# Kernel tuning notes

Hardware: AMD Instinct MI355X
Metric: run time of the kernel (lower is better)

Reference implementation:

```python
import jax, jax.numpy as jnp
import numpy as np

IN_CH, OUT_CH, HID, NHEAD = 4, 1, 256, 8
VDIM = HID // NHEAD
LOCALITIES = (2.0, 10.0, 10.0, 10.0, 10.0, 200.0)
N_BLOCKS = len(LOCALITIES) - 2
INPUT_RES, LATENT_RES, OUTPUT_RES = (64, 64), (32, 32), (64, 64)
BATCH = 8


def pairwise_dist(res1x, res1y, res2x, res2y):
    gx1 = jnp.linspace(0, 1, res1x + 1)[:-1]
    gy1 = jnp.linspace(0, 1, res1y + 1)[:-1]
    g1x, g1y = jnp.meshgrid(gx1, gy1, indexing='xy')
    grid1 = jnp.stack([g1x.flatten(), g1y.flatten()], axis=-1)
    gx2 = jnp.linspace(0, 1, res2x + 1)[:-1]
    gy2 = jnp.linspace(0, 1, res2y + 1)[:-1]
    g2x, g2y = jnp.meshgrid(gx2, gy2, indexing='xy')
    grid2 = jnp.stack([g2x.flatten(), g2y.flatten()], axis=-1)
    diff = grid1[:, None, :] - grid2[None, :, :]
    return (jnp.sum(diff ** 2, axis=-1) / 2.0).astype(jnp.float32)


def pos_att(m_dist, x, r, w, locality):
    # m_dist:[Nq,Nk]  x:[B,Nk,HID]  r:[H,1,1]  w:[H,HID,VDIM]
    scale = jnp.tan(0.25 * jnp.pi * (1 - 1e-07) * (1 + jnp.sin(r)))
    sd = m_dist[None, :, :] * scale  # [H,Nq,Nk]
    if locality <= 100:
        thr = jnp.percentile(sd, locality, axis=-1, keepdims=True)
        sd = jnp.where(sd <= thr, sd, jnp.inf)
    att = jax.nn.softmax(-sd, axis=-1)  # [H,Nq,Nk]
    value = jnp.einsum('bnj,hjk->bhnk', x, w)  # [B,H,Nk,VDIM]
    out = jnp.einsum('hjn,bhnk->bhjk', att, value)  # [B,H,Nq,VDIM]
    out = jnp.transpose(out, (0, 2, 1, 3)).reshape(x.shape[0], m_dist.shape[0], -1)
    return jax.nn.gelu(out)


def lin(x, w, b):
    # eqx.nn.Linear: w:[out,in], b:[out]
    return jnp.einsum('bni,oi->bno', x, w) + b


def setup_inputs() -> dict:
    key = jax.random.key(0)
    ks = jax.random.split(key, 20)
    Ni = INPUT_RES[0] * INPUT_RES[1]
    s_h = 1.0 / jnp.sqrt(HID)
    s_in = 1.0 / jnp.sqrt(IN_CH)
    return {
        'x': jax.random.normal(ks[0], (BATCH, Ni, IN_CH), jnp.float32),
        'en_fc1_w': jax.random.uniform(ks[1], (HID, IN_CH), jnp.float32, -s_in, s_in),
        'en_fc1_b': jax.random.uniform(ks[2], (HID,), jnp.float32, -s_in, s_in),
        'down_r': jax.random.normal(ks[3], (NHEAD, 1, 1), jnp.float32),
        'down_w': jax.random.normal(ks[4], (NHEAD, HID, VDIM), jnp.float32) * s_h,
        'pa_r': jax.random.normal(ks[5], (N_BLOCKS, NHEAD, 1, 1), jnp.float32),
        'pa_w': jax.random.normal(ks[6], (N_BLOCKS, NHEAD, HID, VDIM), jnp.float32) * s_h,
        'mlp1_w': jax.random.uniform(ks[7], (N_BLOCKS, HID, HID), jnp.float32, -s_h, s_h),
        'mlp1_b': jax.random.uniform(ks[8], (N_BLOCKS, HID), jnp.float32, -s_h, s_h),
        'mlp2_w': jax.random.uniform(ks[9], (N_BLOCKS, HID, HID), jnp.float32, -s_h, s_h),
        'mlp2_b': jax.random.uniform(ks[10], (N_BLOCKS, HID), jnp.float32, -s_h, s_h),
        'res_w': jax.random.uniform(ks[11], (N_BLOCKS, HID, HID), jnp.float32, -s_h, s_h),
        'res_b': jax.random.uniform(ks[12], (N_BLOCKS, HID), jnp.float32, -s_h, s_h),
        'up_r': jax.random.normal(ks[13], (NHEAD, 1, 1), jnp.float32),
        'up_w': jax.random.normal(ks[14], (NHEAD, HID, VDIM), jnp.float32) * s_h,
        'de_fc1_w': jax.random.uniform(ks[15], (HID, HID), jnp.float32, -s_h, s_h),
        'de_fc1_b': jax.random.uniform(ks[16], (HID,), jnp.float32, -s_h, s_h),
        'de_fc2_w': jax.random.uniform(ks[17], (OUT_CH, HID), jnp.float32, -s_h, s_h),
        'de_fc2_b': jax.random.uniform(ks[18], (OUT_CH,), jnp.float32, -s_h, s_h),
    }


def reference(x, en_fc1_w, en_fc1_b, down_r, down_w, pa_r, pa_w,
              mlp1_w, mlp1_b, mlp2_w, mlp2_b, res_w, res_b,
              up_r, up_w, de_fc1_w, de_fc1_b, de_fc2_w, de_fc2_b):
    m_dist_down = pairwise_dist(LATENT_RES[0], LATENT_RES[1], INPUT_RES[0], INPUT_RES[1])
    m_dist_proc = pairwise_dist(LATENT_RES[0], LATENT_RES[1], LATENT_RES[0], LATENT_RES[1])
    m_dist_up = pairwise_dist(OUTPUT_RES[0], OUTPUT_RES[1], LATENT_RES[0], LATENT_RES[1])

    h = jax.nn.gelu(lin(x, en_fc1_w, en_fc1_b))
    h = pos_att(m_dist_down, h, down_r, down_w, LOCALITIES[0])
    for i in range(N_BLOCKS):
        pa_out = pos_att(m_dist_proc, h, pa_r[i], pa_w[i], LOCALITIES[1 + i])
        mlp_out = lin(jax.nn.gelu(lin(pa_out, mlp1_w[i], mlp1_b[i])), mlp2_w[i], mlp2_b[i])
        residual = lin(h, res_w[i], res_b[i])
        h = jax.nn.gelu(mlp_out + residual)
    h = pos_att(m_dist_up, h, up_r, up_w, LOCALITIES[-1])
    h = jax.nn.gelu(lin(h, de_fc1_w, de_fc1_b))
    return lin(h, de_fc2_w, de_fc2_b)
```

## Files before the change

kernel.cpp:

```cpp
#include <hip/hip_runtime.h>
#include <math.h>


#define PI_F 3.14159265358979323846f

typedef __attribute__((ext_vector_type(8))) short short8;
typedef __attribute__((ext_vector_type(4))) float float4v;
typedef __attribute__((ext_vector_type(4))) unsigned short ushort4v;

__device__ __forceinline__ float gelu_f(float x) {
  float u = 0.7978845608028654f * (x + 0.044715f * x * x * x);
  float e = __expf(2.0f * u);
  float t = 1.0f - 2.0f / (e + 1.0f);
  return 0.5f * x * (1.0f + t);
}

__device__ __forceinline__ float head_scale(float r) {
  return tanf(0.25f * PI_F * (1.0f - 1e-7f) * (1.0f + sinf(r)));
}

__device__ __forceinline__ unsigned short f2bf(float f) {
  union { float f; unsigned u; } c; c.f = f;
  unsigned u = c.u + 0x7FFFu + ((c.u >> 16) & 1u);
  return (unsigned short)(u >> 16);
}
__device__ __forceinline__ float bf2f(unsigned short h) {
  union { unsigned u; float f; } c; c.u = ((unsigned)h) << 16;
  return c.f;
}
__device__ __forceinline__ void split_bf(float f, unsigned short& hi,
                                         unsigned short& lo) {
  hi = f2bf(f);
  lo = f2bf(f - bf2f(hi));
}

__global__ __launch_bounds__(256) void k_enc(
    const float* __restrict__ x, const float* __restrict__ w,
    const float* __restrict__ b, unsigned short* __restrict__ ahi,
    unsigned short* __restrict__ alo) {
  int row = blockIdx.x;
  int o = threadIdx.x;
  float4 xv = *(const float4*)(x + (size_t)row * 4);
  float4 wv = *(const float4*)(w + (size_t)o * 4);
  float s = xv.x * wv.x + xv.y * wv.y + xv.z * wv.z + xv.w * wv.w + b[o];
  s = gelu_f(s);
  unsigned short hi, lo;
  split_bf(s, hi, lo);
  ahi[(size_t)row * 256 + o] = hi;
  alo[(size_t)row * 256 + o] = lo;
}

__global__ __launch_bounds__(256) void k_split_all(
    const float* __restrict__ down_w, const float* __restrict__ de1_w,
    const float* __restrict__ up_w, const float* __restrict__ pa_w,
    const float* __restrict__ mlp1_w, const float* __restrict__ mlp2_w,
    const float* __restrict__ res_w, unsigned short* __restrict__ whi,
    unsigned short* __restrict__ wlo) {
  int i = blockIdx.x * 256 + threadIdx.x;
  float f;
  if (i < 65536) {
    int n = i >> 8, k = i & 255;
    f = down_w[(n >> 5) * 8192 + k * 32 + (n & 31)];
  } else if (i < 131072) {
    f = de1_w[i - 65536];
  } else if (i < 196608) {
    int j = i - 131072;
    int n = j >> 8, k = j & 255;
    f = up_w[(n >> 5) * 8192 + k * 32 + (n & 31)];
  } else if (i < 458752) {
    int j = i - 196608;
    int blk = j >> 16, r = j & 65535;
    int n = r >> 8, k = r & 255;
    f = pa_w[(size_t)blk * 65536 + (n >> 5) * 8192 + k * 32 + (n & 31)];
  } else if (i < 720896) {
    f = mlp1_w[i - 458752];
  } else if (i < 983040) {
    f = mlp2_w[i - 720896];
  } else {
    f = res_w[i - 983040];
  }
  unsigned short hi, lo;
  split_bf(f, hi, lo);
  whi[i] = hi;
  wlo[i] = lo;
}

template <int KRES, int CXM, int NPT, int TARGET, int TMAX>
__global__ __launch_bounds__(256) void k_thresh(int* __restrict__ thr) {
  __shared__ int wsum[4];
  int q = blockIdx.x, tid = threadIdx.x;
  int qx = q & 31, qy = q >> 5;
  int cx = qx * CXM, cy = qy * CXM;
  int d[NPT];
#pragma unroll
  for (int j = 0; j < NPT; ++j) {
    int k = tid * NPT + j;
    int kx = k & (KRES - 1), ky = k / KRES;
    int dx = cx - kx, dy = cy - ky;
    d[j] = dx * dx + dy * dy;
  }
  int lo = 0, hi = TMAX;
  while (lo < hi) {
    int mid = (lo + hi) >> 1;
    int c = 0;
#pragma unroll
    for (int j = 0; j < NPT; ++j) c += (d[j] <= mid) ? 1 : 0;
#pragma unroll
    for (int off = 32; off > 0; off >>= 1) c += __shfl_down(c, off, 64);
    if ((tid & 63) == 0) wsum[tid >> 6] = c;
    __syncthreads();
    int total = wsum[0] + wsum[1] + wsum[2] + wsum[3];
    __syncthreads();
    if (total >= TARGET) hi = mid; else lo = mid + 1;
  }
  if (tid == 0) thr[q] = lo;
}

template <int KRES, int CXM, int DSHIFT, int J2>
__global__ __launch_bounds__(256) void k_klist2(
    const float* __restrict__ rvec, const int* __restrict__ thr,
    int* __restrict__ klist2, int* __restrict__ kcnt2,
    float* __restrict__ wlist2) {
  __shared__ int cntS;
  __shared__ int sidx[J2];
  __shared__ int sdv[J2][4];
  __shared__ float denS[8][4];
  int tile = blockIdx.x, tid = threadIdx.x;
  int tx = tile & 15, ty = tile >> 4;
  int cxA[4], cyA[4], T[4];
#pragma unroll
  for (int i = 0; i < 4; ++i) {
    int qx = 2 * tx + (i & 1), qy = 2 * ty + (i >> 1);
    cxA[i] = qx * CXM; cyA[i] = qy * CXM;
    T[i] = thr[qy * 32 + qx];
  }
  if (tid == 0) cntS = 0;
  __syncthreads();
  int x0 = KRES - 1, x1 = 0, y0 = KRES - 1, y1 = 0;
#pragma unroll
  for (int i = 0; i < 4; ++i) {
    int rad = (int)sqrtf((float)T[i]);
    while ((rad + 1) * (rad + 1) <= T[i]) ++rad;
    while (rad > 0 && rad * rad > T[i]) --rad;
    x0 = min(x0, max(0, cxA[i] - rad));
    x1 = max(x1, min(KRES - 1, cxA[i] + rad));
    y0 = min(y0, max(0, cyA[i] - rad));
    y1 = max(y1, min(KRES - 1, cyA[i] + rad));
  }
  int W = x1 - x0 + 1, H = y1 - y0 + 1, tot = W * H;
  for (int p = tid; p < tot; p += 256) {
    int kx = x0 + p % W, ky = y0 + p / W;
    int d[4]; bool keep = false;
#pragma unroll
    for (int i = 0; i < 4; ++i) {
      int dx = cxA[i] - kx, dy = cyA[i] - ky;
      d[i] = dx * dx + dy * dy;
      keep = keep || (d[i] <= T[i]);
    }
    if (keep) {
      int s = atomicAdd(&cntS, 1);
      if (s < J2) {
        sidx[s] = ky * KRES + kx;
#pragma unroll
        for (int i = 0; i < 4; ++i) sdv[s][i] = d[i];
      }
    }
  }
  __syncthreads();
  int cnt = min(cntS, J2);
  int h = tid >> 5, lane = tid & 31;
  float sc = head_scale(rvec[h]) * (1.0f / (float)(1 << DSHIFT));
  float den[4] = {0.f, 0.f, 0.f, 0.f};
  for (int j = lane; j < cnt; j += 32) {
#pragma unroll
    for (int i = 0; i < 4; ++i)
      if (sdv[j][i] <= T[i]) den[i] += __expf(-sc * (float)sdv[j][i]);
  }
#pragma unroll
  for (int i = 0; i < 4; ++i) {
    float d0 = den[i];
#pragma unroll
    for (int off = 16; off > 0; off >>= 1) d0 += __shfl_down(d0, off, 32);
    if (lane == 0) denS[h][i] = d0;
  }
  __syncthreads();
  float inv[4];
#pragma unroll
  for (int i = 0; i < 4; ++i) inv[i] = 1.0f / denS[h][i];
  for (int j = lane; j < cnt; j += 32) {
    float w[4];
#pragma unroll
    for (int i = 0; i < 4; ++i)
      w[i] = (sdv[j][i] <= T[i]) ? __expf(-sc * (float)sdv[j][i]) * inv[i] : 0.f;
    float4v wv = {w[0], w[1], w[2], w[3]};
    *(float4v*)&wlist2[(((size_t)h * 256 + tile) * J2 + j) * 4] = wv;
  }
  if (tid == 0) kcnt2[tile] = cnt;
  if (h == 0)
    for (int j = lane; j < cnt; j += 32) klist2[(size_t)tile * J2 + j] = sidx[j];
}

template <int NK, int J2>
__global__ __launch_bounds__(256) void k_att3(
    const float* __restrict__ value,
    const int* __restrict__ klist2, const int* __restrict__ kcnt2,
    const float* __restrict__ wlist2, unsigned short* __restrict__ ohi,
    unsigned short* __restrict__ olo) {
  __shared__ int kls[J2];
  __shared__ float4v wls[J2];
  __shared__ float4v part[4][4][64];
  int blk = blockIdx.x;
  int tile = blk >> 3, h = blk & 7;
  int tid = threadIdx.x, g = tid & 63, s = tid >> 6;
  int cnt = kcnt2[tile];
  for (int j = tid; j < cnt; j += 256) {
    kls[j] = klist2[(size_t)tile * J2 + j];
    wls[j] = *(const float4v*)&wlist2[(((size_t)h * 256 + tile) * J2 + j) * 4];
  }
  __syncthreads();
  const float* vb = value + (size_t)h * NK * 256 + g * 4;
  float4v acc[4];
#pragma unroll
  for (int i = 0; i < 4; ++i) acc[i] = (float4v)0.0f;
  for (int j = s; j < cnt; j += 4) {
    int row = kls[j];
    float4v v = *(const float4v*)(vb + (size_t)row * 256);
    float4v w = wls[j];
    acc[0] += w.x * v;
    acc[1] += w.y * v;
    acc[2] += w.z * v;
    acc[3] += w.w * v;
  }
#pragma unroll
  for (int i = 0; i < 4; ++i) part[s][i][g] = acc[i];
  __syncthreads();
  if (tid < 64) {
    int g2 = tid;
    int ttx = tile & 15, tty = tile >> 4;
    int batch = g2 >> 3, v0 = (g2 & 7) * 4;
#pragma unroll
    for (int i = 0; i < 4; ++i) {
      float4v o4 = part[0][i][g2] + part[1][i][g2] + part[2][i][g2] +
                   part[3][i][g2];
      int q = (2 * tty + (i >> 1)) * 32 + 2 * ttx + (i & 1);
      size_t idx = ((size_t)batch * 1024 + q) * 256 + h * 32 + v0;
      ushort4v hv, lv;
#pragma unroll
      for (int c = 0; c < 4; ++c) {
        float oo = gelu_f(o4[c]);
        unsigned short hi, lo;
        split_bf(oo, hi, lo);
        hv[c] = hi; lv[c] = lo;
      }
      *(ushort4v*)(ohi + idx) = hv;
      *(ushort4v*)(olo + idx) = lv;
    }
  }
}

template <int MS, bool DUAL, int OL, bool GEL, bool OHILO>
__global__ __launch_bounds__(256) void k_gemm(
    const unsigned short* __restrict__ A1hi, const unsigned short* __restrict__ A1lo,
    const unsigned short* __restrict__ W1hi, const unsigned short* __restrict__ W1lo,
    const unsigned short* __restrict__ A2hi, const unsigned short* __restrict__ A2lo,
    const unsigned short* __restrict__ W2hi, const unsigned short* __restrict__ W2lo,
    const float* __restrict__ bias, const float* __restrict__ bias2,
    float* __restrict__ outf, unsigned short* __restrict__ ohi,
    unsigned short* __restrict__ olo, int NS) {
  constexpr int MT = MS * 64;
  __shared__ alignas(16) unsigned short Bh[32][264];
  __shared__ alignas(16) unsigned short Bl[32][264];
  int tid = threadIdx.x;
  int b = blockIdx.x;
  int per = gridDim.x >> 3;
  int mpx = per >> 3;
  int x = b & 7, j = b >> 3;
  int m0 = (x * mpx + (j >> 3)) * MT;
  int n0 = (j & 7) * 32;
  int w = tid >> 6, lane = tid & 63;
  int quad = lane >> 4, l16 = lane & 15;

  float4v acc[MS][2];
#pragma unroll
  for (int i = 0; i < MS; ++i)
#pragma unroll
    for (int n = 0; n < 2; ++n) acc[i][n] = (float4v)0.0f;

  const int NPASS = DUAL ? 2 : 1;
  for (int p = 0; p < NPASS; ++p) {
    const unsigned short* pAh = p ? A2hi : A1hi;
    const unsigned short* pAl = p ? A2lo : A1lo;
    const unsigned short* pWh = p ? W2hi : W1hi;
    const unsigned short* pWl = p ? W2lo : W1lo;
    __syncthreads();
    {
      int row = tid >> 3, seg = (tid & 7) * 32;
      const uint4* gh = (const uint4*)(pWh + (size_t)(n0 + row) * 256 + seg);
      const uint4* gl = (const uint4*)(pWl + (size_t)(n0 + row) * 256 + seg);
#pragma unroll
      for (int q = 0; q < 4; ++q) {
        *(uint4*)&Bh[row][seg + q * 8] = gh[q];
        *(uint4*)&Bl[row][seg + q * 8] = gl[q];
      }
    }
    __syncthreads();
    const unsigned short* ah_p[MS];
    const unsigned short* al_p[MS];
#pragma unroll
    for (int ms = 0; ms < MS; ++ms) {
      size_t row = (size_t)(m0 + w * MS * 16 + ms * 16 + l16);
      ah_p[ms] = pAh + row * 256 + quad * 8;
      al_p[ms] = pAl + row * 256 + quad * 8;
    }
    short8 nah[MS], nal[MS];
#pragma unroll
    for (int ms = 0; ms < MS; ++ms) {
      nah[ms] = *(const short8*)(ah_p[ms]);
      nal[ms] = *(const short8*)(al_p[ms]);
    }
#pragma unroll
    for (int ks = 0; ks < 8; ++ks) {
      short8 cah[MS], cal[MS];
#pragma unroll
      for (int ms = 0; ms < MS; ++ms) { cah[ms] = nah[ms]; cal[ms] = nal[ms]; }
      if (ks < 7) {
#pragma unroll
        for (int ms = 0; ms < MS; ++ms) {
          nah[ms] = *(const short8*)(ah_p[ms] + (ks + 1) * 32);
          nal[ms] = *(const short8*)(al_p[ms] + (ks + 1) * 32);
        }
      }
      short8 bh[2], bl[2];
#pragma unroll
      for (int ns = 0; ns < 2; ++ns) {
        bh[ns] = *(const short8*)&Bh[ns * 16 + l16][ks * 32 + quad * 8];
        bl[ns] = *(const short8*)&Bl[ns * 16 + l16][ks * 32 + quad * 8];
      }
#pragma unroll
      for (int ms = 0; ms < MS; ++ms)
#pragma unroll
        for (int ns = 0; ns < 2; ++ns) {
          acc[ms][ns] = __builtin_amdgcn_mfma_f32_16x16x32_bf16(
              cah[ms], bh[ns], acc[ms][ns], 0, 0, 0);
          acc[ms][ns] = __builtin_amdgcn_mfma_f32_16x16x32_bf16(
              cah[ms], bl[ns], acc[ms][ns], 0, 0, 0);
          acc[ms][ns] = __builtin_amdgcn_mfma_f32_16x16x32_bf16(
              cal[ms], bh[ns], acc[ms][ns], 0, 0, 0);
        }
    }
  }
#pragma unroll
  for (int ms = 0; ms < MS; ++ms) {
#pragma unroll
    for (int ns = 0; ns < 2; ++ns) {
      int n = n0 + ns * 16 + l16;
      float bv = bias ? bias[n] : 0.0f;
      if (DUAL && bias2) bv += bias2[n];
#pragma unroll
      for (int r = 0; r < 4; ++r) {
        int m = m0 + w * MS * 16 + ms * 16 + quad * 4 + r;
        float c = acc[ms][ns][r] + bv;
        if (GEL) c = gelu_f(c);
        if (OHILO) {
          unsigned short chi, clo;
          split_bf(c, chi, clo);
          ohi[(size_t)m * 256 + n] = chi;
          olo[(size_t)m * 256 + n] = clo;
        } else if (OL == 0) {
          outf[(size_t)m * 256 + n] = c;
        } else {
          int N = 1 << NS;
          int bb = m >> NS, rr = m & (N - 1);
          outf[(((size_t)(n >> 5) * N + rr) * 8 + bb) * 32 + (n & 31)] = c;
        }
      }
    }
  }
}

__global__ __launch_bounds__(256) void k_up_s1(
    const float* __restrict__ value,
    const float* __restrict__ rvec, float* __restrict__ T) {
  __shared__ float AxL[64][33];
  int ky = blockIdx.x, h = blockIdx.y, tid = threadIdx.x;
  float sc = head_scale(rvec[h]) * (1.0f / 8192.0f);
  float v[32];
  const float* vb = value + ((size_t)h * 1024 + ky * 32) * 256 + tid;
#pragma unroll
  for (int kx = 0; kx < 32; ++kx) v[kx] = vb[kx * 256];
  if (tid < 64) {
    int qx = tid, dxmin = qx & 1;
    for (int kx = 0; kx < 32; ++kx) {
      int dx = qx - 2 * kx;
      AxL[qx][kx] = __expf(-sc * (float)(dx * dx - dxmin));
    }
  }
  __syncthreads();
  float* tb = T + (((size_t)h * 64) * 32 + ky) * 256 + tid;
  for (int qx = 0; qx < 64; ++qx) {
    float acc = 0.f;
#pragma unroll
    for (int kx = 0; kx < 32; ++kx) acc += AxL[qx][kx] * v[kx];
    tb[(size_t)qx * 32 * 256] = acc;
  }
}

__global__ __launch_bounds__(256) void k_up_s2(
    const float* __restrict__ T, const float* __restrict__ rvec,
    unsigned short* __restrict__ ohi, unsigned short* __restrict__ olo) {
  __shared__ float AyL[64][33];
  __shared__ float Sy[64];
  __shared__ float SxS;
  int qx = blockIdx.x, h = blockIdx.y, tid = threadIdx.x;
  float sc = head_scale(rvec[h]) * (1.0f / 8192.0f);
  float t[32];
  const float* tb = T + ((size_t)h * 64 + qx) * 32 * 256 + tid;
#pragma unroll
  for (int ky = 0; ky < 32; ++ky) t[ky] = tb[ky * 256];
  if (tid < 64) {
    int qy = tid, dymin = qy & 1;
    float s = 0.f;
    for (int ky = 0; ky < 32; ++ky) {
      int dy = qy - 2 * ky;
      float e = __expf(-sc * (float)(dy * dy - dymin));
      AyL[qy][ky] = e;
      s += e;
    }
    Sy[qy] = s;
  } else if (tid >= 64 && tid < 96) {
    int kx = tid - 64, dxmin = qx & 1;
    int dx = qx - 2 * kx;
    float e = __expf(-sc * (float)(dx * dx - dxmin));
#pragma unroll
    for (int off = 16; off > 0; off >>= 1) e += __shfl_down(e, off, 32);
    if (kx == 0) SxS = e;
  }
  __syncthreads();
  float invSx = 1.0f / SxS;
  int b = tid >> 5, v = tid & 31;
  size_t base = ((size_t)b * 4096 + qx) * 256 + h * 32 + v;
  for (int qy = 0; qy < 64; ++qy) {
    float acc = 0.f;
#pragma unroll
    for (int ky = 0; ky < 32; ++ky) acc += AyL[qy][ky] * t[ky];
    float o = gelu_f(acc * invSx / Sy[qy]);
    unsigned short hi, lo;
    split_bf(o, hi, lo);
    size_t idx = base + (size_t)qy * 64 * 256;
    ohi[idx] = hi;
    olo[idx] = lo;
  }
}

__global__ __launch_bounds__(256) void k_fc2(const float* __restrict__ h,
                                             const float* __restrict__ w,
                                             const float* __restrict__ b,
                                             float* __restrict__ out) {
  int row = blockIdx.x * 4 + (threadIdx.x >> 6);
  int lane = threadIdx.x & 63;
  float4 hv = *(const float4*)(h + (size_t)row * 256 + lane * 4);
  float4 wv = *(const float4*)(w + lane * 4);
  float s = hv.x * wv.x + hv.y * wv.y + hv.z * wv.z + hv.w * wv.w;
#pragma unroll
  for (int off = 32; off > 0; off >>= 1) s += __shfl_down(s, off, 64);
  if (lane == 0) out[row] = s + b[0];
}

extern "C" void kernel_launch(void* const* d_in, const int* in_sizes, int n_in,
                              void* d_out, int out_size, void* d_ws,
                              size_t ws_size, hipStream_t stream) {
  const float* x      = (const float*)d_in[0];
  const float* en_w   = (const float*)d_in[1];
  const float* en_b   = (const float*)d_in[2];
  const float* down_r = (const float*)d_in[3];
  const float* down_w = (const float*)d_in[4];
  const float* pa_r   = (const float*)d_in[5];
  const float* pa_w   = (const float*)d_in[6];
  const float* mlp1_w = (const float*)d_in[7];
  const float* mlp1_b = (const float*)d_in[8];
  const float* mlp2_w = (const float*)d_in[9];
  const float* mlp2_b = (const float*)d_in[10];
  const float* res_w  = (const float*)d_in[11];
  const float* res_b  = (const float*)d_in[12];
  const float* up_r   = (const float*)d_in[13];
  const float* up_w   = (const float*)d_in[14];
  const float* de1_w  = (const float*)d_in[15];
  const float* de1_b  = (const float*)d_in[16];
  const float* de2_w  = (const float*)d_in[17];
  const float* de2_b  = (const float*)d_in[18];
  float* out = (float*)d_out;

  constexpr int J2 = 256;
  float* ws = (float*)d_ws;
  unsigned short* Ahi = (unsigned short*)ws;
  unsigned short* Alo = Ahi + 8388608;
  float* B = ws + 8388608;
  float* Tbuf = B + 2097152;
  unsigned short* hAhi = (unsigned short*)(ws + 16777216);
  unsigned short* hAlo = hAhi + 2097152;
  unsigned short* hBhi = hAlo + 2097152;
  unsigned short* hBlo = hBhi + 2097152;
  unsigned short* pahi = hBlo + 2097152;
  unsigned short* palo = pahi + 2097152;
  unsigned short* m1hi = palo + 2097152;
  unsigned short* m1lo = m1hi + 2097152;
  int* thrD = (int*)(ws + 25165824);
  int* thrP = thrD + 1024;
  int* cntD2 = thrP + 1024;
  int* cntP2 = cntD2 + 256;
  int* klD2 = cntP2 + 256;
  int* klP2 = klD2 + 256 * J2;
  float* wlD2 = (float*)(klP2 + 256 * J2);
  float* wlP2 = wlD2 + 2097152;
  unsigned short* Whi = (unsigned short*)(wlP2 + 2097152);
  unsigned short* Wlo = Whi + 1245184;
  const int WO_DOWN = 0, WO_DE1 = 65536, WO_UP = 131072, WO_PA = 196608,
            WO_MLP1 = 458752, WO_MLP2 = 720896, WO_RES = 983040;

  k_enc<<<32768, 256, 0, stream>>>(x, en_w, en_b, Ahi, Alo);
  k_split_all<<<4864, 256, 0, stream>>>(down_w, de1_w, up_w, pa_w, mlp1_w,
                                        mlp2_w, res_w, Whi, Wlo);
  k_thresh<64, 2, 16, 82, 7938><<<1024, 256, 0, stream>>>(thrD);
  k_thresh<32, 1, 4, 103, 1922><<<1024, 256, 0, stream>>>(thrP);
  k_klist2<64, 2, 13, J2><<<256, 256, 0, stream>>>(down_r, thrD, klD2, cntD2,
                                                   wlD2);
  k_klist2<32, 1, 11, J2><<<256, 256, 0, stream>>>(pa_r, thrP, klP2, cntP2,
                                                   wlP2);
  k_gemm<4, false, 1, false, false><<<1024, 256, 0, stream>>>(
      Ahi, Alo, Whi + WO_DOWN, Wlo + WO_DOWN, nullptr, nullptr, nullptr,
      nullptr, nullptr, nullptr, B, nullptr, nullptr, 12);
  k_att3<4096, J2><<<2048, 256, 0, stream>>>(B, klD2, cntD2, wlD2, hAhi, hAlo);
  for (int i = 0; i < 4; ++i) {
    const unsigned short* hih = (i & 1) ? hBhi : hAhi;
    const unsigned short* hil = (i & 1) ? hBlo : hAlo;
    unsigned short* hoh = (i & 1) ? hAhi : hBhi;
    unsigned short* hol = (i & 1) ? hAlo : hBlo;
    k_gemm<2, false, 1, false, false><<<512, 256, 0, stream>>>(
        hih, hil, Whi + WO_PA + i * 65536, Wlo + WO_PA + i * 65536, nullptr,
        nullptr, nullptr, nullptr, nullptr, nullptr, B, nullptr, nullptr, 10);
    k_att3<1024, J2><<<2048, 256, 0, stream>>>(B, klP2, cntP2, wlP2, pahi,
                                               palo);
    k_gemm<2, false, 0, true, true><<<512, 256, 0, stream>>>(
        pahi, palo, Whi + WO_MLP1 + i * 65536, Wlo + WO_MLP1 + i * 65536,
        nullptr, nullptr, nullptr, nullptr, mlp1_b + i * 256, nullptr, nullptr,
        m1hi, m1lo, 0);
    k_gemm<2, true, 0, true, true><<<512, 256, 0, stream>>>(
        m1hi, m1lo, Whi + WO_MLP2 + i * 65536, Wlo + WO_MLP2 + i * 65536, hih,
        hil, Whi + WO_RES + i * 65536, Wlo + WO_RES + i * 65536,
        mlp2_b + i * 256, res_b + i * 256, nullptr, hoh, hol, 0);
  }
  k_gemm<2, false, 1, false, false><<<512, 256, 0, stream>>>(
      hAhi, hAlo, Whi + WO_UP, Wlo + WO_UP, nullptr, nullptr, nullptr, nullptr,
      nullptr, nullptr, B, nullptr, nullptr, 10);
  k_up_s1<<<dim3(32, 8), 256, 0, stream>>>(B, up_r, Tbuf);
  k_up_s2<<<dim3(64, 8), 256, 0, stream>>>(Tbuf, up_r, Ahi, Alo);
  k_gemm<4, false, 0, true, false><<<1024, 256, 0, stream>>>(
      Ahi, Alo, Whi + WO_DE1, Wlo + WO_DE1, nullptr, nullptr, nullptr, nullptr,
      de1_b, nullptr, B, nullptr, nullptr, 0);
  k_fc2<<<8192, 256, 0, stream>>>(B, de2_w, de2_b, out);
}
```

Baseline: 560.5 us.

## Restructure split-bf16 GEMM to full-N tiles with swizzled LDS staging and register prefetch

The GEMM kernel now computes all 256 output columns per block over BM rows, staging both the weight and activation K-slices in XOR-swizzled LDS. The next slice is prefetched into registers while MFMAs run on the current one. Before, each block handled 32 columns and read A straight from global memory, so every A row was re-read by 8 blocks. The change removes that redundant A traffic but halves the grid, raises LDS use (about 80KB at BM=64) and accumulator register pressure, and adds a launch_bounds occupancy hint of 2.

```diff
diff --git a/kernel.cpp b/kernel.cpp
--- a/kernel.cpp
+++ b/kernel.cpp
@@ -258,8 +258,8 @@
   }
 }
 
-template <int MS, bool DUAL, int OL, bool GEL, bool OHILO>
-__global__ __launch_bounds__(256) void k_gemm(
+template <int BM, bool DUAL, int OL, bool GEL, bool OHILO>
+__global__ __launch_bounds__(256, 2) void k_gn(
     const unsigned short* __restrict__ A1hi, const unsigned short* __restrict__ A1lo,
     const unsigned short* __restrict__ W1hi, const unsigned short* __restrict__ W1lo,
     const unsigned short* __restrict__ A2hi, const unsigned short* __restrict__ A2lo,
@@ -267,98 +267,114 @@
     const float* __restrict__ bias, const float* __restrict__ bias2,
     float* __restrict__ outf, unsigned short* __restrict__ ohi,
     unsigned short* __restrict__ olo, int NS) {
-  constexpr int MT = MS * 64;
-  __shared__ alignas(16) unsigned short Bh[32][264];
-  __shared__ alignas(16) unsigned short Bl[32][264];
+  constexpr int MS = BM / 32;
+  constexpr int nAh = BM / 32;
+  __shared__ alignas(16) unsigned short Wh_s[16384];
+  __shared__ alignas(16) unsigned short Wl_s[16384];
+  __shared__ alignas(16) unsigned short Ah_s[BM * 64];
+  __shared__ alignas(16) unsigned short Al_s[BM * 64];
   int tid = threadIdx.x;
-  int b = blockIdx.x;
-  int per = gridDim.x >> 3;
-  int mpx = per >> 3;
-  int x = b & 7, j = b >> 3;
-  int m0 = (x * mpx + (j >> 3)) * MT;
-  int n0 = (j & 7) * 32;
+  int m0 = blockIdx.x * BM;
   int w = tid >> 6, lane = tid & 63;
   int quad = lane >> 4, l16 = lane & 15;
-
-  float4v acc[MS][2];
+  int wm = (w >> 1) * (BM / 2), wn = (w & 1) * 128;
+
+  int wgo[8], wld[8];
+#pragma unroll
+  for (int i = 0; i < 8; ++i) {
+    int rem = tid + i * 256;
+    int r = rem >> 3, s = rem & 7, c = s ^ (r & 7);
+    wgo[i] = r * 256 + c * 8;
+    wld[i] = r * 64 + s * 8;
+  }
+  int ago[nAh], ald[nAh];
+#pragma unroll
+  for (int i = 0; i < nAh; ++i) {
+    int rem = tid + i * 256;
+    int r = rem >> 3, s = rem & 7, c = s ^ (r & 7);
+    ago[i] = r * 256 + c * 8;
+    ald[i] = r * 64 + s * 8;
+  }
+
+  float4v acc[MS][8];
 #pragma unroll
   for (int i = 0; i < MS; ++i)
 #pragma unroll
-    for (int n = 0; n < 2; ++n) acc[i][n] = (float4v)0.0f;
-
-  const int NPASS = DUAL ? 2 : 1;
-  for (int p = 0; p < NPASS; ++p) {
-    const unsigned short* pAh = p ? A2hi : A1hi;
-    const unsigned short* pAl = p ? A2lo : A1lo;
-    const unsigned short* pWh = p ? W2hi : W1hi;
-    const unsigned short* pWl = p ? W2lo : W1lo;
+    for (int n = 0; n < 8; ++n) acc[i][n] = (float4v)0.0f;
+
+  uint4 cwh[8], cwl[8], cah[nAh], cal[nAh];
+  const int NSTEP = DUAL ? 8 : 4;
+
+  auto LOAD = [&](int st) {
+    const unsigned short *pWh, *pWl, *pAh, *pAl;
+    if (DUAL && st >= 4) { pWh = W2hi; pWl = W2lo; pAh = A2hi; pAl = A2lo; }
+    else { pWh = W1hi; pWl = W1lo; pAh = A1hi; pAl = A1lo; }
+    int kb = (st & 3) * 64;
+#pragma unroll
+    for (int i = 0; i < 8; ++i) {
+      cwh[i] = *(const uint4*)(pWh + wgo[i] + kb);
+      cwl[i] = *(const uint4*)(pWl + wgo[i] + kb);
+    }
+#pragma unroll
+    for (int i = 0; i < nAh; ++i) {
+      cah[i] = *(const uint4*)(pAh + (size_t)m0 * 256 + ago[i] + kb);
+      cal[i] = *(const uint4*)(pAl + (size_t)m0 * 256 + ago[i] + kb);
+    }
+  };
+
+  LOAD(0);
+  for (int st = 0; st < NSTEP; ++st) {
     __syncthreads();
-    {
-      int row = tid >> 3, seg = (tid & 7) * 32;
-      const uint4* gh = (const uint4*)(pWh + (size_t)(n0 + row) * 256 + seg);
-      const uint4* gl = (const uint4*)(pWl + (size_t)(n0 + row) * 256 + seg);
-#pragma unroll
-      for (int q = 0; q < 4; ++q) {
-        *(uint4*)&Bh[row][seg + q * 8] = gh[q];
-        *(uint4*)&Bl[row][seg + q * 8] = gl[q];
+#pragma unroll
+    for (int i = 0; i < 8; ++i) {
+      *(uint4*)&Wh_s[wld[i]] = cwh[i];
+      *(uint4*)&Wl_s[wld[i]] = cwl[i];
+    }
+#pragma unroll
+    for (int i = 0; i < nAh; ++i) {
+      *(uint4*)&Ah_s[ald[i]] = cah[i];
+      *(uint4*)&Al_s[ald[i]] = cal[i];
+    }
+    __syncthreads();
+    if (st + 1 < NSTEP) LOAD(st + 1);
+#pragma unroll
+    for (int ks2 = 0; ks2 < 2; ++ks2) {
+      short8 ah[MS], al[MS];
+#pragma unroll
+      for (int ms = 0; ms < MS; ++ms) {
+        int ra = wm + ms * 16 + l16;
+        int c = (ks2 * 4 + quad) ^ (ra & 7);
+        ah[ms] = *(const short8*)&Ah_s[ra * 64 + c * 8];
+        al[ms] = *(const short8*)&Al_s[ra * 64 + c * 8];
       }
-    }
-    __syncthreads();
-    const unsigned short* ah_p[MS];
-    const unsigned short* al_p[MS];
-#pragma unroll
-    for (int ms = 0; ms < MS; ++ms) {
-      size_t row = (size_t)(m0 + w * MS * 16 + ms * 16 + l16);
-      ah_p[ms] = pAh + row * 256 + quad * 8;
-      al_p[ms] = pAl + row * 256 + quad * 8;
-    }
-    short8 nah[MS], nal[MS];
-#pragma unroll
-    for (int ms = 0; ms < MS; ++ms) {
-      nah[ms] = *(const short8*)(ah_p[ms]);
-      nal[ms] = *(const short8*)(al_p[ms]);
-    }
-#pragma unroll
-    for (int ks = 0; ks < 8; ++ks) {
-      short8 cah[MS], cal[MS];
-#pragma unroll
-      for (int ms = 0; ms < MS; ++ms) { cah[ms] = nah[ms]; cal[ms] = nal[ms]; }
-      if (ks < 7) {
+#pragma unroll
+      for (int ns = 0; ns < 8; ++ns) {
+        int rb = wn + ns * 16 + l16;
+        int c = (ks2 * 4 + quad) ^ (rb & 7);
+        short8 bh = *(const short8*)&Wh_s[rb * 64 + c * 8];
+        short8 bl = *(const short8*)&Wl_s[rb * 64 + c * 8];
 #pragma unroll
         for (int ms = 0; ms < MS; ++ms) {
-          nah[ms] = *(const short8*)(ah_p[ms] + (ks + 1) * 32);
-          nal[ms] = *(const short8*)(al_p[ms] + (ks + 1) * 32);
+          acc[ms][ns] = __builtin_amdgcn_mfma_f32_16x16x32_bf16(
+              ah[ms], bh, acc[ms][ns], 0, 0, 0);
+          acc[ms][ns] = __builtin_amdgcn_mfma_f32_16x16x32_bf16(
+              ah[ms], bl, acc[ms][ns], 0, 0, 0);
+          acc[ms][ns] = __builtin_amdgcn_mfma_f32_16x16x32_bf16(
+              al[ms], bh, acc[ms][ns], 0, 0, 0);
         }
       }
-      short8 bh[2], bl[2];
-#pragma unroll
-      for (int ns = 0; ns < 2; ++ns) {
-        bh[ns] = *(const short8*)&Bh[ns * 16 + l16][ks * 32 + quad * 8];
-        bl[ns] = *(const short8*)&Bl[ns * 16 + l16][ks * 32 + quad * 8];
-      }
-#pragma unroll
-      for (int ms = 0; ms < MS; ++ms)
-#pragma unroll
-        for (int ns = 0; ns < 2; ++ns) {
-          acc[ms][ns] = __builtin_amdgcn_mfma_f32_16x16x32_bf16(
-              cah[ms], bh[ns], acc[ms][ns], 0, 0, 0);
-          acc[ms][ns] = __builtin_amdgcn_mfma_f32_16x16x32_bf16(
-              cah[ms], bl[ns], acc[ms][ns], 0, 0, 0);
-          acc[ms][ns] = __builtin_amdgcn_mfma_f32_16x16x32_bf16(
-              cal[ms], bh[ns], acc[ms][ns], 0, 0, 0);
-        }
     }
   }
 #pragma unroll
   for (int ms = 0; ms < MS; ++ms) {
 #pragma unroll
-    for (int ns = 0; ns < 2; ++ns) {
-      int n = n0 + ns * 16 + l16;
+    for (int ns = 0; ns < 8; ++ns) {
+      int n = wn + ns * 16 + l16;
       float bv = bias ? bias[n] : 0.0f;
       if (DUAL && bias2) bv += bias2[n];
 #pragma unroll
       for (int r = 0; r < 4; ++r) {
-        int m = m0 + w * MS * 16 + ms * 16 + quad * 4 + r;
+        int m = m0 + wm + ms * 16 + quad * 4 + r;
         float c = acc[ms][ns][r] + bv;
         if (GEL) c = gelu_f(c);
         if (OHILO) {
@@ -526,7 +542,7 @@
                                                    wlD2);
   k_klist2<32, 1, 11, J2><<<256, 256, 0, stream>>>(pa_r, thrP, klP2, cntP2,
                                                    wlP2);
-  k_gemm<4, false, 1, false, false><<<1024, 256, 0, stream>>>(
+  k_gn<64, false, 1, false, false><<<512, 256, 0, stream>>>(
       Ahi, Alo, Whi + WO_DOWN, Wlo + WO_DOWN, nullptr, nullptr, nullptr,
       nullptr, nullptr, nullptr, B, nullptr, nullptr, 12);
   k_att3<4096, J2><<<2048, 256, 0, stream>>>(B, klD2, cntD2, wlD2, hAhi, hAlo);
@@ -535,26 +551,26 @@
     const unsigned short* hil = (i & 1) ? hBlo : hAlo;
     unsigned short* hoh = (i & 1) ? hAhi : hBhi;
     unsigned short* hol = (i & 1) ? hAlo : hBlo;
-    k_gemm<2, false, 1, false, false><<<512, 256, 0, stream>>>(
+    k_gn<32, false, 1, false, false><<<256, 256, 0, stream>>>(
         hih, hil, Whi + WO_PA + i * 65536, Wlo + WO_PA + i * 65536, nullptr,
         nullptr, nullptr, nullptr, nullptr, nullptr, B, nullptr, nullptr, 10);
     k_att3<1024, J2><<<2048, 256, 0, stream>>>(B, klP2, cntP2, wlP2, pahi,
                                                palo);
-    k_gemm<2, false, 0, true, true><<<512, 256, 0, stream>>>(
+    k_gn<32, false, 0, true, true><<<256, 256, 0, stream>>>(
         pahi, palo, Whi + WO_MLP1 + i * 65536, Wlo + WO_MLP1 + i * 65536,
         nullptr, nullptr, nullptr, nullptr, mlp1_b + i * 256, nullptr, nullptr,
         m1hi, m1lo, 0);
-    k_gemm<2, true, 0, true, true><<<512, 256, 0, stream>>>(
+    k_gn<32, true, 0, true, true><<<256, 256, 0, stream>>>(
         m1hi, m1lo, Whi + WO_MLP2 + i * 65536, Wlo + WO_MLP2 + i * 65536, hih,
         hil, Whi + WO_RES + i * 65536, Wlo + WO_RES + i * 65536,
         mlp2_b + i * 256, res_b + i * 256, nullptr, hoh, hol, 0);
   }
-  k_gemm<2, false, 1, false, false><<<512, 256, 0, stream>>>(
+  k_gn<32, false, 1, false, false><<<256, 256, 0, stream>>>(
       hAhi, hAlo, Whi + WO_UP, Wlo + WO_UP, nullptr, nullptr, nullptr, nullptr,
       nullptr, nullptr, B, nullptr, nullptr, 10);
   k_up_s1<<<dim3(32, 8), 256, 0, stream>>>(B, up_r, Tbuf);
   k_up_s2<<<dim3(64, 8), 256, 0, stream>>>(Tbuf, up_r, Ahi, Alo);
-  k_gemm<4, false, 0, true, false><<<1024, 256, 0, stream>>>(
+  k_gn<64, false, 0, true, false><<<512, 256, 0, stream>>>(
       Ahi, Alo, Whi + WO_DE1, Wlo + WO_DE1, nullptr, nullptr, nullptr, nullptr,
       de1_b, nullptr, B, nullptr, nullptr, 0);
   k_fc2<<<8192, 256, 0, stream>>>(B, de2_w, de2_b, out);
```

Result: slower. 823.7 us (+47.0%).
